# Performance work log

Hardware: AMD Instinct MI355X
Metric: run time of the kernel (lower is better)

Reference implementation:

```python
import jax, jax.numpy as jnp
import numpy as np

RADIUS = 0.3      # extents/2, extents = radius_scale*6*particle_radius = 4*6*0.025 = 0.6
KSIZE = 4         # kernel_size [4,4,4]
KMAX = 80         # padded neighbor count
N = 50000
BOX = 5.2         # box side -> ~40 neighbors within RADIUS on average
CIN = 3
COUT = 3
_PI = 3.14159265358979323846


def _build_neighbors(pos, radius, kmax):
    # fixed-radius search (L2), ignore_query_point=True, padded to kmax per row
    n = pos.shape[0]
    r2 = radius * radius
    sq = (pos * pos).sum(1)
    idx = np.zeros((n, kmax), np.int32)
    msk = np.zeros((n, kmax), np.bool_)
    ch = 2500
    for s in range(0, n, ch):
        e = min(s + ch, n)
        d2 = sq[s:e, None] + sq[None, :] - 2.0 * (pos[s:e] @ pos.T)
        d2[np.arange(e - s), np.arange(s, e)] = np.inf  # radius_search_ignore_query_points
        rows, cols = np.nonzero(d2 < r2)
        starts = np.searchsorted(rows, np.arange(e - s))
        slot = np.arange(len(rows)) - starts[rows]
        keep = slot < kmax
        idx[rows[keep] + s, slot[keep]] = cols[keep]
        msk[rows[keep] + s, slot[keep]] = True
    return idx, msk


def setup_inputs():
    key = jax.random.key(0)
    k1, k2, k3 = jax.random.split(key, 3)
    pos = jax.random.uniform(k1, (N, 3), jnp.float32) * BOX
    vel = jax.random.normal(k2, (N, 3), jnp.float32)
    # keras 'uniform' initializer: U(-0.05, 0.05)
    kernel = jax.random.uniform(k3, (KSIZE, KSIZE, KSIZE, CIN, COUT), jnp.float32, -0.05, 0.05)
    nidx, nmask = _build_neighbors(np.asarray(pos), RADIUS, KMAX)
    return {"pos": pos, "vel": vel, "kernel": kernel,
            "neighbor_idx": jnp.asarray(nidx), "neighbor_mask": jnp.asarray(nmask)}


def _ball_to_cube_volume_preserving(u):
    # Open3D CoordinateTransformation.h: MapSphereToCylinder then MapCylinderToCube
    eps = 1e-12
    x, y, z = u[..., 0], u[..., 1], u[..., 2]
    sq = x * x + y * y + z * z
    norm = jnp.sqrt(jnp.maximum(sq, eps))
    sq_xy = x * x + y * y
    # sphere -> cylinder
    top = (1.25 * z * z) > sq_xy
    s_top = jnp.sqrt(3.0 * norm / (norm + jnp.abs(z)))
    s_side = norm / jnp.sqrt(jnp.maximum(sq_xy, eps))
    x1 = jnp.where(top, x * s_top, x * s_side)
    y1 = jnp.where(top, y * s_top, y * s_side)
    z1 = jnp.where(top, jnp.sign(z) * norm, 1.5 * z)
    small = sq < eps
    x1 = jnp.where(small, x, x1)
    y1 = jnp.where(small, y, y1)
    z1 = jnp.where(small, z, z1)
    # cylinder -> cube (equal-area disc->square on xy)
    sq_xy1 = x1 * x1 + y1 * y1
    norm_xy = jnp.sqrt(jnp.maximum(sq_xy1, eps))
    xbig = jnp.abs(y1) <= jnp.abs(x1)
    sx = jnp.sign(x1) * norm_xy
    sy = jnp.sign(y1) * norm_xy
    safe_x = jnp.where(jnp.abs(x1) > eps, x1, 1.0)
    safe_y = jnp.where(jnp.abs(y1) > eps, y1, 1.0)
    x2 = jnp.where(xbig, sx, sy * (4.0 / _PI) * jnp.arctan(x1 / safe_y))
    y2 = jnp.where(xbig, sx * (4.0 / _PI) * jnp.arctan(y1 / safe_x), sy)
    small_xy = sq_xy1 < eps
    x2 = jnp.where(small_xy, x1, x2)
    y2 = jnp.where(small_xy, y1, y2)
    return x2, y2, z1


def _grid_coords(c):
    # align_corners=True: [-1,1] -> [0, KSIZE-1]; 'linear' interpolation clamps to border
    t = jnp.clip((c + 1.0) * (0.5 * (KSIZE - 1)), 0.0, KSIZE - 1.0)
    t0 = jnp.floor(t)
    i0 = t0.astype(jnp.int32)
    i1 = jnp.minimum(i0 + 1, KSIZE - 1)
    f = t - t0
    return (i0, i1), (1.0 - f, f)


def _cconv(pos, vel, kernel, neighbor_idx, neighbor_mask):
    n = pos.shape[0]
    rel = pos[neighbor_idx] - pos[:, None, :]              # [N,K,3]
    d2 = jnp.sum(rel * rel, -1)
    # window_poly6 on squared distance normalized by radius^2
    imp = jnp.clip((1.0 - d2 / (RADIUS * RADIUS)) ** 3, 0.0, 1.0)
    imp = imp * neighbor_mask.astype(vel.dtype)
    cx, cy, cz = _ball_to_cube_volume_preserving(rel / RADIUS)
    (xi0, xi1), (wx0, wx1) = _grid_coords(cx)
    (yi0, yi1), (wy0, wy1) = _grid_coords(cy)
    (zi0, zi1), (wz0, wz1) = _grid_coords(cz)
    phi = vel[neighbor_idx] * imp[..., None]               # [N,K,Cin]
    rows = jnp.arange(n)[:, None]
    # accumulate window*trilinear-weighted features into the 64 filter taps,
    # then contract once with the flattened kernel (math identical to per-pair
    # interp(W) @ feat since everything is linear)
    A = jnp.zeros((n, KSIZE * KSIZE * KSIZE, vel.shape[1]), vel.dtype)
    for zi, wz in ((zi0, wz0), (zi1, wz1)):
        for yi, wy in ((yi0, wy0), (yi1, wy1)):
            for xi, wx in ((xi0, wx0), (xi1, wx1)):
                corner = (zi * KSIZE + yi) * KSIZE + xi
                A = A.at[rows, corner].add((wz * wy * wx)[..., None] * phi)
    Wflat = kernel.reshape(KSIZE * KSIZE * KSIZE, kernel.shape[3], kernel.shape[4])
    return jnp.einsum('ngi,gio->no', A, Wflat)        # [N, COUT]


def reference(pos, vel, kernel, neighbor_idx, neighbor_mask):
    return _cconv(pos, vel, kernel, neighbor_idx, neighbor_mask)
```

## Files before the change

### kernel.cpp

```cpp
#include <hip/hip_runtime.h>
#include <math.h>

#define N_PART 50000
#define KMAX 80
#define KS 4
#define LPP 16

typedef __attribute__((ext_vector_type(8))) _Float16 h8;
typedef __attribute__((ext_vector_type(2))) _Float16 h2;

__device__ __forceinline__ float atan_poly(float t) {
    float t2 = t * t;
    float p = -0.01172120f;
    p = p * t2 + 0.05265332f;
    p = p * t2 - 0.11643287f;
    p = p * t2 + 0.19354346f;
    p = p * t2 - 0.33262347f;
    p = p * t2 + 0.99997726f;
    return t * p;
}

struct PV { float px, py, pz, ux, uy, uz; };

__device__ __forceinline__ void load_pv(const float* __restrict__ pos,
                                        const float* __restrict__ vel,
                                        int i, PV& v) {
    v.px = pos[3*i];  v.py = pos[3*i+1];  v.pz = pos[3*i+2];
    v.ux = vel[3*i];  v.uy = vel[3*i+1];  v.uz = vel[3*i+2];
}

__device__ __forceinline__ void pair_contrib(
    const PV& n, float cpx, float cpy, float cpz,
    const _Float16* __restrict__ WsHP,
    float& acc0, float& acc1, float& acc2)
{
    const float inv_r = 1.0f / 0.3f;
    const float eps   = 1e-12f;
    const float FOUR_OVER_PI = 1.27323954473516268615f;

    float rx = (n.px - cpx) * inv_r;
    float ry = (n.py - cpy) * inv_r;
    float rz = (n.pz - cpz) * inv_r;

    float sq = rx * rx + ry * ry + rz * rz;

    float t1  = 1.0f - sq;
    float imp = fmaxf(t1 * t1 * t1, 0.0f);

    float norm   = sqrtf(fmaxf(sq, eps));
    float sq_xy  = rx * rx + ry * ry;
    bool  top    = (1.25f * rz * rz) > sq_xy;
    float rsq_xy = __builtin_amdgcn_rsqf(fmaxf(sq_xy, eps));
    float s_top  = sqrtf(3.0f * norm * __builtin_amdgcn_rcpf(norm + fabsf(rz)));
    float z1 = top ? copysignf(norm, rz) : 1.5f * rz;

    float nxy = top ? (sq_xy * rsq_xy * s_top) : norm;
    bool  xb  = fabsf(ry) <= fabsf(rx);
    float num = xb ? ry : rx;
    float den = xb ? rx : ry;
    float sden = (fabsf(den) > eps) ? den : 1.0f;
    float t    = num * __builtin_amdgcn_rcpf(sden);
    float at   = atan_poly(t);
    float sd   = copysignf(nxy, den);
    float u    = sd * FOUR_OVER_PI * at;
    float x2   = xb ? sd : u;
    float y2   = xb ? u  : sd;

    float tx = fminf(fmaxf(x2 * 1.5f + 1.5f, 0.0f), 3.0f);
    float ty = fminf(fmaxf(y2 * 1.5f + 1.5f, 0.0f), 3.0f);
    float tz = fminf(fmaxf(z1 * 1.5f + 1.5f, 0.0f), 3.0f);
    int xi0 = (int)tx, yi0 = (int)ty, zi0 = (int)tz;
    float wx1 = __builtin_amdgcn_fractf(tx);
    float wy1 = __builtin_amdgcn_fractf(ty);
    float wz1 = __builtin_amdgcn_fractf(tz);
    int xi1 = min(xi0 + 1, KS - 1);
    int yi1 = min(yi0 + 1, KS - 1);
    int zi1 = min(zi0 + 1, KS - 1);
    float wx0 = 1.0f - wx1, wy0 = 1.0f - wy1, wz0 = 1.0f - wz1;

    int   zia[2] = { zi0 << 4, zi1 << 4 };  float wza[2] = { wz0, wz1 };
    int   yia[2] = { yi0 << 2, yi1 << 2 };  float wya[2] = { wy0, wy1 };
    int   xia[2] = { xi0, xi1 };            float wxa[2] = { wx0, wx1 };

    h2 M01 = (h2)(_Float16)0.0f;
    h2 M23 = (h2)(_Float16)0.0f;
    h2 M45 = (h2)(_Float16)0.0f;
    h2 M67 = (h2)(_Float16)0.0f;
    h2 M89 = (h2)(_Float16)0.0f;

    #pragma unroll
    for (int cz = 0; cz < 2; ++cz) {
        #pragma unroll
        for (int cy = 0; cy < 2; ++cy) {
            float wzy = wza[cz] * wya[cy];
            int   czy = zia[cz] + yia[cy];
            #pragma unroll
            for (int cx = 0; cx < 2; ++cx) {
                int corner = czy + xia[cx];
                const _Float16* Wc = &WsHP[corner << 4];
                h8 lo = *(const h8*)Wc;
                h2 hi = *(const h2*)(Wc + 8);
                float wf = wzy * wxa[cx];
                _Float16 wh = (_Float16)wf;
                h2 ww = { wh, wh };
                M01 += ww * __builtin_shufflevector(lo, lo, 0, 1);
                M23 += ww * __builtin_shufflevector(lo, lo, 2, 3);
                M45 += ww * __builtin_shufflevector(lo, lo, 4, 5);
                M67 += ww * __builtin_shufflevector(lo, lo, 6, 7);
                M89 += ww * hi;
            }
        }
    }

    float m0 = (float)M01[0], m1 = (float)M01[1];
    float m2 = (float)M23[0], m3 = (float)M23[1];
    float m4 = (float)M45[0], m5 = (float)M45[1];
    float m6 = (float)M67[0], m7 = (float)M67[1];
    float m8 = (float)M89[0];
    float s0 = n.ux * m0 + n.uy * m3 + n.uz * m6;
    float s1 = n.ux * m1 + n.uy * m4 + n.uz * m7;
    float s2 = n.ux * m2 + n.uy * m5 + n.uz * m8;
    acc0 += imp * s0;
    acc1 += imp * s1;
    acc2 += imp * s2;
}

__global__ __launch_bounds__(256) void cconv_kernel(
    const float* __restrict__ pos,
    const float* __restrict__ vel,
    const float* __restrict__ Wg,
    const int* __restrict__ nidx,
    const void* __restrict__ nmask,
    float* __restrict__ out)
{
    __shared__ _Float16 WsHP[64 * 16];
    for (int t = threadIdx.x; t < 64 * 16; t += blockDim.x) {
        int g = t >> 4, r = t & 15;
        WsHP[t] = (r < 9) ? (_Float16)Wg[g * 9 + r] : (_Float16)0.0f;
    }
    __syncthreads();

    int gid = blockIdx.x * blockDim.x + threadIdx.x;
    int p   = gid >> 4;
    int sub = gid & 15;

    const int base = p * KMAX;

    int idxs[5];
    #pragma unroll
    for (int m = 0; m < 5; ++m)
        idxs[m] = nidx[base + sub + (m << 4)];

    bool byteMask;
    {
        const unsigned* mw = (const unsigned*)nmask;
        int lane = threadIdx.x & 63;
        bool big = false;
        #pragma unroll
        for (int i = 0; i < 8; ++i)
            big |= (mw[lane + 64 * i] > 1u);
        byteMask = (__ballot(big) != 0ULL);
    }

    float cpx = pos[3 * p], cpy = pos[3 * p + 1], cpz = pos[3 * p + 2];

    int lc = 0;
    if (byteMask) {
        const unsigned char* mb = (const unsigned char*)nmask;
        #pragma unroll
        for (int m = 0; m < 5; ++m) lc += (mb[base + sub + (m << 4)] != 0);
    } else {
        const int* mi = (const int*)nmask;
        #pragma unroll
        for (int m = 0; m < 5; ++m) lc += (mi[base + sub + (m << 4)] != 0);
    }
    lc += __shfl_xor(lc, 1); lc += __shfl_xor(lc, 2);
    lc += __shfl_xor(lc, 4); lc += __shfl_xor(lc, 8);
    const int cnt = lc;

    PV A, An;
    load_pv(pos, vel, idxs[0], A);

    float acc0 = 0.0f, acc1 = 0.0f, acc2 = 0.0f;

    int m = 0;
    for (int k = sub; k < cnt; k += LPP) {
        int mn = min(m + 1, 4);
        load_pv(pos, vel, idxs[mn], An);

        pair_contrib(A, cpx, cpy, cpz, WsHP, acc0, acc1, acc2);

        A = An; ++m;
    }

    acc0 += __shfl_xor(acc0, 1); acc0 += __shfl_xor(acc0, 2);
    acc0 += __shfl_xor(acc0, 4); acc0 += __shfl_xor(acc0, 8);
    acc1 += __shfl_xor(acc1, 1); acc1 += __shfl_xor(acc1, 2);
    acc1 += __shfl_xor(acc1, 4); acc1 += __shfl_xor(acc1, 8);
    acc2 += __shfl_xor(acc2, 1); acc2 += __shfl_xor(acc2, 2);
    acc2 += __shfl_xor(acc2, 4); acc2 += __shfl_xor(acc2, 8);

    if (sub == 0) {
        out[p * 3 + 0] = acc0;
        out[p * 3 + 1] = acc1;
        out[p * 3 + 2] = acc2;
    }
}

extern "C" void kernel_launch(void* const* d_in, const int* in_sizes, int n_in,
                              void* d_out, int out_size, void* d_ws, size_t ws_size,
                              hipStream_t stream) {
    const float* pos   = (const float*)d_in[0];
    const float* vel   = (const float*)d_in[1];
    const float* Wg    = (const float*)d_in[2];
    const int*   nidx  = (const int*)d_in[3];
    const void*  nmask = d_in[4];
    float*       out   = (float*)d_out;

    int threads = 256;
    long long total = (long long)N_PART * LPP;
    int grid = (int)((total + threads - 1) / threads);
    cconv_kernel<<<grid, threads, 0, stream>>>(pos, vel, Wg, nidx, nmask, out);
}
```

Measured before the change: 29.52 us.

## Use 8 lanes per particle with rolling neighbor-index prefetch and fused sqrt

Each particle now gets 8 lanes instead of 16, so every lane handles about 5 neighbors instead of 2-3. This halves the grid and shortens the cross-lane reductions. The five upfront neighbor-index loads become a two-deep rolling prefetch of the index 16 slots ahead. The top-branch sqrt/rsq pair is folded into a single sqrt. The cost is a longer serial loop per lane, more dependent latency, and fewer waves to hide memory stalls.

```diff
diff --git a/kernel.cpp b/kernel.cpp
--- a/kernel.cpp
+++ b/kernel.cpp
@@ -4,7 +4,7 @@
 #define N_PART 50000
 #define KMAX 80
 #define KS 4
-#define LPP 16
+#define LPP 8
 
 typedef __attribute__((ext_vector_type(8))) _Float16 h8;
 typedef __attribute__((ext_vector_type(2))) _Float16 h2;
@@ -47,14 +47,13 @@
     float t1  = 1.0f - sq;
     float imp = fmaxf(t1 * t1 * t1, 0.0f);
 
-    float norm   = sqrtf(fmaxf(sq, eps));
-    float sq_xy  = rx * rx + ry * ry;
-    bool  top    = (1.25f * rz * rz) > sq_xy;
-    float rsq_xy = __builtin_amdgcn_rsqf(fmaxf(sq_xy, eps));
-    float s_top  = sqrtf(3.0f * norm * __builtin_amdgcn_rcpf(norm + fabsf(rz)));
-    float z1 = top ? copysignf(norm, rz) : 1.5f * rz;
-
-    float nxy = top ? (sq_xy * rsq_xy * s_top) : norm;
+    float norm  = sqrtf(fmaxf(sq, eps));
+    float sq_xy = rx * rx + ry * ry;
+    bool  top   = (1.25f * rz * rz) > sq_xy;
+    float z1    = top ? copysignf(norm, rz) : 1.5f * rz;
+
+    float nxy = top ? sqrtf(sq_xy * 3.0f * norm * __builtin_amdgcn_rcpf(norm + fabsf(rz)))
+                    : norm;
     bool  xb  = fabsf(ry) <= fabsf(rx);
     float num = xb ? ry : rx;
     float den = xb ? rx : ry;
@@ -141,15 +140,11 @@
     __syncthreads();
 
     int gid = blockIdx.x * blockDim.x + threadIdx.x;
-    int p   = gid >> 4;
-    int sub = gid & 15;
+    int p   = gid >> 3;
+    int sub = gid & 7;
+    if (p >= N_PART) return;
 
     const int base = p * KMAX;
-
-    int idxs[5];
-    #pragma unroll
-    for (int m = 0; m < 5; ++m)
-        idxs[m] = nidx[base + sub + (m << 4)];
 
     bool byteMask;
     {
@@ -168,37 +163,33 @@
     if (byteMask) {
         const unsigned char* mb = (const unsigned char*)nmask;
         #pragma unroll
-        for (int m = 0; m < 5; ++m) lc += (mb[base + sub + (m << 4)] != 0);
+        for (int m = 0; m < 10; ++m) lc += (mb[base + sub + (m << 3)] != 0);
     } else {
         const int* mi = (const int*)nmask;
         #pragma unroll
-        for (int m = 0; m < 5; ++m) lc += (mi[base + sub + (m << 4)] != 0);
-    }
-    lc += __shfl_xor(lc, 1); lc += __shfl_xor(lc, 2);
-    lc += __shfl_xor(lc, 4); lc += __shfl_xor(lc, 8);
+        for (int m = 0; m < 10; ++m) lc += (mi[base + sub + (m << 3)] != 0);
+    }
+    lc += __shfl_xor(lc, 1); lc += __shfl_xor(lc, 2); lc += __shfl_xor(lc, 4);
     const int cnt = lc;
 
+    int idxA = nidx[base + sub];
+    int idxB = nidx[base + sub + 8];
+
     PV A, An;
-    load_pv(pos, vel, idxs[0], A);
+    load_pv(pos, vel, idxA, A);
 
     float acc0 = 0.0f, acc1 = 0.0f, acc2 = 0.0f;
 
-    int m = 0;
     for (int k = sub; k < cnt; k += LPP) {
-        int mn = min(m + 1, 4);
-        load_pv(pos, vel, idxs[mn], An);
-
+        int idxC = nidx[base + min(k + 16, KMAX - 1)];
+        load_pv(pos, vel, idxB, An);
         pair_contrib(A, cpx, cpy, cpz, WsHP, acc0, acc1, acc2);
-
-        A = An; ++m;
-    }
-
-    acc0 += __shfl_xor(acc0, 1); acc0 += __shfl_xor(acc0, 2);
-    acc0 += __shfl_xor(acc0, 4); acc0 += __shfl_xor(acc0, 8);
-    acc1 += __shfl_xor(acc1, 1); acc1 += __shfl_xor(acc1, 2);
-    acc1 += __shfl_xor(acc1, 4); acc1 += __shfl_xor(acc1, 8);
-    acc2 += __shfl_xor(acc2, 1); acc2 += __shfl_xor(acc2, 2);
-    acc2 += __shfl_xor(acc2, 4); acc2 += __shfl_xor(acc2, 8);
+        idxB = idxC; A = An;
+    }
+
+    acc0 += __shfl_xor(acc0, 1); acc0 += __shfl_xor(acc0, 2); acc0 += __shfl_xor(acc0, 4);
+    acc1 += __shfl_xor(acc1, 1); acc1 += __shfl_xor(acc1, 2); acc1 += __shfl_xor(acc1, 4);
+    acc2 += __shfl_xor(acc2, 1); acc2 += __shfl_xor(acc2, 2); acc2 += __shfl_xor(acc2, 4);
 
     if (sub == 0) {
         out[p * 3 + 0] = acc0;
```

Measured after the change: 33.55 us. 13.7% more time.
